# Kernel tuning notes

Hardware: AMD Instinct MI355X
Metric: run time of the kernel (lower is better)

Reference implementation:

```python
import math
import jax, jax.numpy as jnp
import numpy as np

T = 4096
D_MODEL = 1024
NUM_HEADS = 16
HEAD_DIM = D_MODEL // NUM_HEADS


def setup_inputs() -> dict:
    key = jax.random.key(0)
    k_x, k_wqkv, k_wproj = jax.random.split(key, 3)
    # match eqx.nn.Linear init scale: U(-1/sqrt(in), 1/sqrt(in)); randn*small works too,
    # but keep magnitudes reasonable so softmax isn't saturated.
    s_in = 1.0 / math.sqrt(D_MODEL)
    x = jax.random.normal(k_x, (T, D_MODEL), dtype=jnp.float32)
    W_qkv = jax.random.normal(k_wqkv, (3 * D_MODEL, D_MODEL), dtype=jnp.float32) * s_in
    b_qkv = jnp.zeros((3 * D_MODEL,), dtype=jnp.float32)
    W_proj = jax.random.normal(k_wproj, (D_MODEL, D_MODEL), dtype=jnp.float32) * s_in
    b_proj = jnp.zeros((D_MODEL,), dtype=jnp.float32)
    return {"x": x, "W_qkv": W_qkv, "b_qkv": b_qkv, "W_proj": W_proj, "b_proj": b_proj}


def reference(x, W_qkv, b_qkv, W_proj, b_proj):
    T_, C = x.shape  # (seq, d_model)
    H, hd = NUM_HEADS, HEAD_DIM
    # c_attn: eqx Linear computes W @ x + b per token -> x @ W.T + b
    qkv = x @ W_qkv.T + b_qkv  # (T, 3C)
    q, k, v = jnp.split(qkv, 3, axis=1)
    # (T, C) -> (H, T, hd)
    q = q.reshape(T_, H, hd).swapaxes(0, 1)
    k = k.reshape(T_, H, hd).swapaxes(0, 1)
    v = v.reshape(T_, H, hd).swapaxes(0, 1)
    scores = jnp.einsum("htd,hsd->hts", q, k) / math.sqrt(hd)  # (H, T, T)
    causal = jnp.tril(jnp.ones((T_, T_), dtype=bool))
    scores = jnp.where(causal, scores, -jnp.inf)
    attn = jax.nn.softmax(scores, axis=-1)
    y = jnp.einsum("hts,hsd->htd", attn, v)  # (H, T, hd)
    y = y.swapaxes(0, 1).reshape(T_, C)
    y = y @ W_proj.T + b_proj
    return y
```

## Files before the change

kernel.cpp:

```cpp
#include <hip/hip_runtime.h>
#include <math.h>
#include <string.h>

#define T_SEQ 4096
#define DM 1024
#define NH 16
#define HD 64

typedef short s8v __attribute__((ext_vector_type(8)));
typedef float f4v __attribute__((ext_vector_type(4)));

__device__ inline unsigned short f2bf(float f) {
    unsigned u; memcpy(&u, &f, 4);
    u = u + 0x7fffu + ((u >> 16) & 1u);
    return (unsigned short)(u >> 16);
}

__device__ inline float bf2f(unsigned short s) {
    unsigned u = (unsigned)s << 16;
    float f; memcpy(&f, &u, 4);
    return f;
}

__device__ inline float exp2fn(float x) {
#if __has_builtin(__builtin_amdgcn_exp2f)
    return __builtin_amdgcn_exp2f(x);
#else
    return exp2f(x);
#endif
}

__device__ inline void gld_lds16(const void* g, void* l) {
    __builtin_amdgcn_global_load_lds(
        (const __attribute__((address_space(1))) void*)g,
        (__attribute__((address_space(3))) void*)l, 16, 0, 0);
}

__global__ __launch_bounds__(256)
void cvt3(const float* __restrict__ i0, unsigned short* __restrict__ o0, int n0,
          const float* __restrict__ i1, unsigned short* __restrict__ o1, int n1,
          const float* __restrict__ i2, unsigned short* __restrict__ o2, int n2) {
    int i = blockIdx.x * 256 + threadIdx.x;
    const float* in; unsigned short* out; int j;
    if (i < n0)           { in = i0; out = o0; j = i; }
    else if (i < n0 + n1) { in = i1; out = o1; j = i - n0; }
    else if (i < n0 + n1 + n2) { in = i2; out = o2; j = i - n0 - n1; }
    else return;
    const float4* p = (const float4*)(in + (size_t)j * 8);
    float4 a = p[0], b = p[1];
    unsigned short o[8] = {f2bf(a.x), f2bf(a.y), f2bf(a.z), f2bf(a.w),
                           f2bf(b.x), f2bf(b.y), f2bf(b.z), f2bf(b.w)};
    uint4 pk; memcpy(&pk, o, 16);
    *(uint4*)(out + (size_t)j * 8) = pk;
}

template<int MODE, int TN>
__global__ __launch_bounds__(256)
void gemm_bt_mfma(const unsigned short* __restrict__ A, const unsigned short* __restrict__ B,
                  const float* __restrict__ bias, void* __restrict__ Cout,
                  unsigned short* __restrict__ qbuf, unsigned short* __restrict__ kbuf2,
                  unsigned short* __restrict__ vT,
                  int M, int N, int K) {
    constexpr int NF = TN / 32;
    __shared__ __align__(16) short As[4096];
    __shared__ __align__(16) short Bs[TN * 32];
    const int tid = threadIdx.x;
    const int w = tid >> 6, lane = tid & 63;
    const int wr = w >> 1, wc = w & 1;
    const int m0 = blockIdx.y * 128, n0 = blockIdx.x * TN;

    const bool doA = (w < 2);
    const bool doStage = doA || ((w & 1) * 64 < TN);
    const unsigned short* src = doA ? A : B;
    const int rbase = (doA ? m0 : n0) + (w & 1) * 64;
    const unsigned short* gsrc = src + (size_t)(rbase + (lane & 15)) * K + ((lane >> 4) * 8);
    short* ldst = (doA ? As : Bs) + ((w & 1) * 4) * 512;

    f4v acc[4][NF];
    #pragma unroll
    for (int i = 0; i < 4; ++i)
        #pragma unroll
        for (int j = 0; j < NF; ++j) acc[i][j] = (f4v){0.f, 0.f, 0.f, 0.f};

    for (int k0 = 0; k0 < K; k0 += 32) {
        __syncthreads();
        if (doStage) {
            #pragma unroll
            for (int i = 0; i < 4; ++i)
                gld_lds16(gsrc + (size_t)(i * 16) * K + k0, ldst + i * 512);
        }
        __syncthreads();

        s8v af[4], bf[NF];
        #pragma unroll
        for (int i = 0; i < 4; ++i) af[i] = *(const s8v*)&As[((wr * 4 + i) * 64 + lane) * 8];
        #pragma unroll
        for (int j = 0; j < NF; ++j) bf[j] = *(const s8v*)&Bs[((wc * NF + j) * 64 + lane) * 8];
        #pragma unroll
        for (int i = 0; i < 4; ++i)
            #pragma unroll
            for (int j = 0; j < NF; ++j)
                acc[i][j] = __builtin_amdgcn_mfma_f32_16x16x32_bf16(af[i], bf[j], acc[i][j], 0, 0, 0);
    }

    const int l15 = lane & 15, quad = lane >> 4;
    float bj[NF];
    #pragma unroll
    for (int j = 0; j < NF; ++j) bj[j] = bias[n0 + wc * (TN / 2) + j * 16 + l15];

    if (MODE == 2 && n0 >= 2 * DM) {
        const int tile = (m0 + wr * 64) >> 6;
        const int hh = ((n0 - 2 * DM) >> 6) + wc;
        #pragma unroll
        for (int i = 0; i < 4; ++i) {
            #pragma unroll
            for (int j = 0; j < NF; ++j) {
                unsigned short o[4];
                #pragma unroll
                for (int rg = 0; rg < 4; ++rg) o[rg] = f2bf(acc[i][j][rg] + bj[j]);
                unsigned long long pk; memcpy(&pk, o, 8);
                size_t off = (size_t)hh * 262144 + (size_t)tile * 4096
                           + (size_t)((j * 2 + (i >> 1)) * 64 + lane) * 8 + (i & 1) * 4;
                *(unsigned long long*)&vT[off] = pk;
            }
        }
    } else if (MODE == 2) {
        unsigned short* dst = (n0 < DM) ? qbuf : kbuf2;
        const int nb = (n0 < DM) ? n0 : n0 - DM;
        #pragma unroll
        for (int i = 0; i < 4; ++i) {
            #pragma unroll
            for (int rg = 0; rg < 4; ++rg) {
                int row = m0 + wr * 64 + i * 16 + quad * 4 + rg;
                #pragma unroll
                for (int j = 0; j < NF; ++j) {
                    int col = nb + wc * (TN / 2) + j * 16 + l15;
                    dst[(size_t)row * DM + col] = f2bf(acc[i][j][rg] + bj[j]);
                }
            }
        }
    } else {
        #pragma unroll
        for (int i = 0; i < 4; ++i) {
            #pragma unroll
            for (int rg = 0; rg < 4; ++rg) {
                int row = m0 + wr * 64 + i * 16 + quad * 4 + rg;
                #pragma unroll
                for (int j = 0; j < NF; ++j) {
                    int col = n0 + wc * (TN / 2) + j * 16 + l15;
                    ((float*)Cout)[(size_t)row * N + col] = acc[i][j][rg] + bj[j];
                }
            }
        }
    }
}

__device__ __forceinline__ void soft_step(f4v* st, bool diag, int qloc, int quad,
                                          float& lr, s8v& pf0, s8v& pf1) {
    const float C2  = 0.1803368851f;
    const float MC2 = 12.0f * 0.1803368851f;
    float sv[4][4];
    #pragma unroll
    for (int kb = 0; kb < 4; ++kb)
        #pragma unroll
        for (int rg = 0; rg < 4; ++rg) {
            float s = st[kb][rg];
            if (diag && (kb * 16 + quad * 4 + rg > qloc)) s = -3.0e38f;
            float t = exp2fn(fmaf(s, C2, -MC2));
            sv[kb][rg] = t;
            lr += t;
        }
    int pk[4][2];
    #pragma unroll
    for (int kb = 0; kb < 4; ++kb) {
        unsigned u0 = __float_as_uint(sv[kb][0]) + 0x8000u;
        unsigned u1 = __float_as_uint(sv[kb][1]) + 0x8000u;
        unsigned u2 = __float_as_uint(sv[kb][2]) + 0x8000u;
        unsigned u3 = __float_as_uint(sv[kb][3]) + 0x8000u;
        pk[kb][0] = (int)__builtin_amdgcn_perm(u1, u0, 0x07060302);
        pk[kb][1] = (int)__builtin_amdgcn_perm(u3, u2, 0x07060302);
    }
    int4 a = {pk[0][0], pk[0][1], pk[1][0], pk[1][1]};
    int4 b = {pk[2][0], pk[2][1], pk[3][0], pk[3][1]};
    memcpy(&pf0, &a, 16);
    memcpy(&pf1, &b, 16);
}

__global__ __launch_bounds__(256, 3)
void attn_mfma7(const unsigned short* __restrict__ qb,
                const unsigned short* __restrict__ kbf,
                const unsigned short* __restrict__ vT,
                unsigned short* __restrict__ y0,
                unsigned short* __restrict__ y1,
                unsigned short* __restrict__ y2,
                float* __restrict__ lsum) {
    const int b = blockIdx.x;
    const int par = b % 3;
    const int idx = b / 3;
    const int h = idx & 15, a = idx >> 4;
    const int tid = threadIdx.x;
    const int w = tid >> 6, lane = tid & 63;
    const int quad = lane >> 4, l15 = lane & 15;
    const int cq = h * HD;
    unsigned short* ypar = (par == 0) ? y0 : (par == 1) ? y1 : y2;
    float* lpar = lsum + ((size_t)par * NH + h) * T_SEQ;
    const unsigned short* vbase = vT + (size_t)h * 262144;

    __shared__ short KB[2][4096];
    __shared__ short VTs[2][4096];
    __shared__ short QB[8192];

    for (int ph = 0; ph < 2; ++ph) {
        const int qt = ph ? (31 - a) : a;
        const int q0 = qt * 128;
        const int kmax = 2 * qt + 1;
        const int nk = (kmax >= par) ? (kmax - par) / 3 + 1 : 0;
        const int kt0 = par * 64;

        __syncthreads();
        #pragma unroll
        for (int rr = 0; rr < 4; ++rr) {
            int ch = rr * 256 + tid;
            int qg = ch >> 7, hf = (ch >> 6) & 1, ln = ch & 63;
            gld_lds16(qb + (size_t)(q0 + qg * 16 + (ln & 15)) * DM + cq + hf * 32 + ((ln >> 4) << 3),
                      &QB[(ch & ~63) * 8]);
        }
        if (nk > 0) {
            #pragma unroll
            for (int rr = 0; rr < 2; ++rr) {
                int ch = rr * 256 + tid;
                int blk = ch >> 7, hf = (ch >> 6) & 1, ln = ch & 63;
                gld_lds16(kbf + (size_t)(kt0 + blk * 16 + (ln & 15)) * DM + cq + hf * 32 + ((ln >> 4) << 3),
                          &KB[0][(ch & ~63) * 8]);
                gld_lds16(vbase + (size_t)(kt0 >> 6) * 4096 + (size_t)ch * 8,
                          &VTs[0][(ch & ~63) * 8]);
            }
        }
        __syncthreads();

        s8v qf[2][2];
        #pragma unroll
        for (int g = 0; g < 2; ++g)
            #pragma unroll
            for (int hf = 0; hf < 2; ++hf)
                qf[g][hf] = *(const s8v*)&QB[((((g * 4 + w) * 2 + hf) * 64) + lane) * 8];

        f4v O0[4], O1[4];
        #pragma unroll
        for (int ob = 0; ob < 4; ++ob) {
            O0[ob] = (f4v){0.f, 0.f, 0.f, 0.f};
            O1[ob] = (f4v){0.f, 0.f, 0.f, 0.f};
        }
        float lr0 = 0.f, lr1 = 0.f;

        for (int i = 0; i < nk; ++i) {
            const int kt = par + 3 * i;
            const int p = i & 1;
            const bool g0a = (kt <= 2 * qt);
            const bool m0 = (kt == 2 * qt);
            const bool m1 = (kt == 2 * qt + 1);
            if (i < nk - 1) {
                const int k1 = kt0 + (i + 1) * 192;
                #pragma unroll
                for (int rr = 0; rr < 2; ++rr) {
                    int ch = rr * 256 + tid;
                    int blk = ch >> 7, hf = (ch >> 6) & 1, ln = ch & 63;
                    gld_lds16(kbf + (size_t)(k1 + blk * 16 + (ln & 15)) * DM + cq
                                  + hf * 32 + ((ln >> 4) << 3),
                              &KB[p ^ 1][(ch & ~63) * 8]);
                    gld_lds16(vbase + (size_t)(k1 >> 6) * 4096 + (size_t)ch * 8,
                              &VTs[p ^ 1][(ch & ~63) * 8]);
                }
            }

            f4v st0[4], st1[4];
            #pragma unroll
            for (int kb = 0; kb < 4; ++kb) {
                s8v k0f = *(const s8v*)&KB[p][((kb * 2 + 0) * 64 + lane) * 8];
                s8v k1f = *(const s8v*)&KB[p][((kb * 2 + 1) * 64 + lane) * 8];
                f4v c1 = (f4v){0.f, 0.f, 0.f, 0.f};
                c1 = __builtin_amdgcn_mfma_f32_16x16x32_bf16(k0f, qf[1][0], c1, 0, 0, 0);
                c1 = __builtin_amdgcn_mfma_f32_16x16x32_bf16(k1f, qf[1][1], c1, 0, 0, 0);
                st1[kb] = c1;
                if (g0a) {
                    f4v c0 = (f4v){0.f, 0.f, 0.f, 0.f};
                    c0 = __builtin_amdgcn_mfma_f32_16x16x32_bf16(k0f, qf[0][0], c0, 0, 0, 0);
                    c0 = __builtin_amdgcn_mfma_f32_16x16x32_bf16(k1f, qf[0][1], c0, 0, 0, 0);
                    st0[kb] = c0;
                }
            }

            s8v pf10, pf11, pf00, pf01;
            soft_step(st1, m1, w * 16 + l15, quad, lr1, pf10, pf11);
            if (g0a) soft_step(st0, m0, w * 16 + l15, quad, lr0, pf00, pf01);

            #pragma unroll
            for (int ob = 0; ob < 4; ++ob) {
                s8v v0f = *(const s8v*)&VTs[p][((ob * 2 + 0) * 64 + lane) * 8];
                s8v v1f = *(const s8v*)&VTs[p][((ob * 2 + 1) * 64 + lane) * 8];
                O1[ob] = __builtin_amdgcn_mfma_f32_16x16x32_bf16(v0f, pf10, O1[ob], 0, 0, 0);
                O1[ob] = __builtin_amdgcn_mfma_f32_16x16x32_bf16(v1f, pf11, O1[ob], 0, 0, 0);
                if (g0a) {
                    O0[ob] = __builtin_amdgcn_mfma_f32_16x16x32_bf16(v0f, pf00, O0[ob], 0, 0, 0);
                    O0[ob] = __builtin_amdgcn_mfma_f32_16x16x32_bf16(v1f, pf01, O0[ob], 0, 0, 0);
                }
            }
            __syncthreads();
        }

        lr0 += __shfl_xor(lr0, 16); lr0 += __shfl_xor(lr0, 32);
        lr1 += __shfl_xor(lr1, 16); lr1 += __shfl_xor(lr1, 32);
        #pragma unroll
        for (int g = 0; g < 2; ++g) {
            const f4v* O = g ? O1 : O0;
            int qrow = q0 + g * 64 + w * 16 + l15;
            size_t ybase = (size_t)qrow * DM + cq;
            #pragma unroll
            for (int ob = 0; ob < 4; ++ob) {
                unsigned short o[4];
                #pragma unroll
                for (int rg = 0; rg < 4; ++rg) o[rg] = f2bf(O[ob][rg]);
                unsigned long long pk; memcpy(&pk, o, 8);
                *(unsigned long long*)&ypar[ybase + ob * 16 + quad * 4] = pk;
            }
            if (quad == 0) lpar[qrow] = g ? lr1 : lr0;
        }
    }
}

__global__ __launch_bounds__(256)
void attn_combine3(const unsigned short* __restrict__ y0,
                   const unsigned short* __restrict__ y1,
                   const unsigned short* __restrict__ y2,
                   const float* __restrict__ lsum,
                   unsigned short* __restrict__ yout) {
    int i = blockIdx.x * 256 + threadIdx.x;
    int t = i >> 7, d8 = i & 127;
    int h = d8 >> 3;
    float l = lsum[(size_t)h * T_SEQ + t]
            + lsum[((size_t)NH + h) * T_SEQ + t]
            + lsum[((size_t)2 * NH + h) * T_SEQ + t];
    float inv = 1.f / l;
    size_t off = (size_t)t * DM + d8 * 8;
    uint4 ua = *(const uint4*)(y0 + off);
    uint4 ub = *(const uint4*)(y1 + off);
    uint4 uc = *(const uint4*)(y2 + off);
    const unsigned short* pa = (const unsigned short*)&ua;
    const unsigned short* pb = (const unsigned short*)&ub;
    const unsigned short* pc = (const unsigned short*)&uc;
    unsigned short o[8];
    #pragma unroll
    for (int k = 0; k < 8; ++k)
        o[k] = f2bf((bf2f(pa[k]) + bf2f(pb[k]) + bf2f(pc[k])) * inv);
    uint4 pk; memcpy(&pk, o, 16);
    *(uint4*)(yout + off) = pk;
}

extern "C" void kernel_launch(void* const* d_in, const int* in_sizes, int n_in,
                              void* d_out, int out_size, void* d_ws, size_t ws_size,
                              hipStream_t stream) {
    const float* x     = (const float*)d_in[0];
    const float* Wqkv  = (const float*)d_in[1];
    const float* bqkv  = (const float*)d_in[2];
    const float* Wproj = (const float*)d_in[3];
    const float* bproj = (const float*)d_in[4];
    float* out = (float*)d_out;

    char* ws = (char*)d_ws;
    unsigned short* qbuf  = (unsigned short*)(ws);
    unsigned short* kbuf  = (unsigned short*)(ws + ( 8u << 20));
    unsigned short* vTb   = (unsigned short*)(ws + (16u << 20));
    unsigned short* yattb = (unsigned short*)(ws + (24u << 20));
    unsigned short* wprjb = (unsigned short*)(ws + (32u << 20));
    float*          lsum  = (float*)         (ws + (34u << 20));
    unsigned short* xb    = (unsigned short*)(ws + (35u << 20));
    unsigned short* wqkvb = (unsigned short*)(ws + (43u << 20));
    unsigned short* y0p   = (unsigned short*)(ws + (35u << 20));
    unsigned short* y1p   = (unsigned short*)(ws + (43u << 20));
    unsigned short* y2p   = (unsigned short*)(ws + (51u << 20));

    dim3 blk(256);
    {
        int n0 = T_SEQ * DM / 8, n1 = 3 * DM * DM / 8, n2 = DM * DM / 8;
        cvt3<<<dim3((n0 + n1 + n2 + 255) / 256), blk, 0, stream>>>(
            x, xb, n0, Wqkv, wqkvb, n1, Wproj, wprjb, n2);
    }
    gemm_bt_mfma<2, 128><<<dim3(3 * DM / 128, T_SEQ / 128), blk, 0, stream>>>(
        xb, wqkvb, bqkv, nullptr, qbuf, kbuf, vTb, T_SEQ, 3 * DM, DM);
    attn_mfma7<<<dim3(768), blk, 0, stream>>>(qbuf, kbuf, vTb, y0p, y1p, y2p, lsum);
    attn_combine3<<<dim3(T_SEQ * DM / 8 / 256), blk, 0, stream>>>(y0p, y1p, y2p, lsum, yattb);
    gemm_bt_mfma<0, 64><<<dim3(DM / 64, T_SEQ / 128), blk, 0, stream>>>(
        yattb, wprjb, bproj, out, nullptr, nullptr, nullptr, T_SEQ, DM, DM);
}
```

Before: 219.5 us.

## Split attention keys four ways, double-buffer GEMM LDS, compute row sums via MFMA

Several changes land together. The GEMM K-loop now double-buffers its LDS tiles, so the next global-to-LDS load overlaps the current MFMAs and the loop needs one fewer barrier per step. Attention splits each head's keys across four partitions instead of three, giving 1024 blocks, and raises the occupancy hint to 4. Q fragments are now read straight from global memory instead of through LDS, and softmax row sums come from an MFMA against a ones vector rather than scalar adds plus shuffles. The combine kernel sums four partial outputs and writes in place over y0, which costs an extra partial buffer and one more read per element in the combine step.

Result: slower. 251.0 us (+14.4%).

```diff
diff --git a/kernel.cpp b/kernel.cpp
--- a/kernel.cpp
+++ b/kernel.cpp
@@ -62,8 +62,8 @@
                   unsigned short* __restrict__ vT,
                   int M, int N, int K) {
     constexpr int NF = TN / 32;
-    __shared__ __align__(16) short As[4096];
-    __shared__ __align__(16) short Bs[TN * 32];
+    __shared__ __align__(16) short As[2][4096];
+    __shared__ __align__(16) short Bs[2][TN * 32];
     const int tid = threadIdx.x;
     const int w = tid >> 6, lane = tid & 63;
     const int wr = w >> 1, wc = w & 1;
@@ -74,7 +74,7 @@
     const unsigned short* src = doA ? A : B;
     const int rbase = (doA ? m0 : n0) + (w & 1) * 64;
     const unsigned short* gsrc = src + (size_t)(rbase + (lane & 15)) * K + ((lane >> 4) * 8);
-    short* ldst = (doA ? As : Bs) + ((w & 1) * 4) * 512;
+    const int ldoff = ((w & 1) * 4) * 512;
 
     f4v acc[4][NF];
     #pragma unroll
@@ -82,25 +82,34 @@
         #pragma unroll
         for (int j = 0; j < NF; ++j) acc[i][j] = (f4v){0.f, 0.f, 0.f, 0.f};
 
-    for (int k0 = 0; k0 < K; k0 += 32) {
+    auto stage = [&](short* base, int k0) {
+        short* ldst = base + ldoff;
+        #pragma unroll
+        for (int i = 0; i < 4; ++i)
+            gld_lds16(gsrc + (size_t)(i * 16) * K + k0, ldst + i * 512);
+    };
+    auto compute = [&](const short* Ab, const short* Bb) {
+        s8v af[4], bfr[NF];
+        #pragma unroll
+        for (int i = 0; i < 4; ++i) af[i] = *(const s8v*)&Ab[((wr * 4 + i) * 64 + lane) * 8];
+        #pragma unroll
+        for (int j = 0; j < NF; ++j) bfr[j] = *(const s8v*)&Bb[((wc * NF + j) * 64 + lane) * 8];
+        #pragma unroll
+        for (int i = 0; i < 4; ++i)
+            #pragma unroll
+            for (int j = 0; j < NF; ++j)
+                acc[i][j] = __builtin_amdgcn_mfma_f32_16x16x32_bf16(af[i], bfr[j], acc[i][j], 0, 0, 0);
+    };
+
+    if (doStage) stage(doA ? As[0] : Bs[0], 0);
+    __syncthreads();
+    for (int k0 = 0; k0 < K; k0 += 64) {
+        if (doStage) stage(doA ? As[1] : Bs[1], k0 + 32);
+        compute(As[0], Bs[0]);
         __syncthreads();
-        if (doStage) {
-            #pragma unroll
-            for (int i = 0; i < 4; ++i)
-                gld_lds16(gsrc + (size_t)(i * 16) * K + k0, ldst + i * 512);
-        }
+        if (doStage && (k0 + 64 < K)) stage(doA ? As[0] : Bs[0], k0 + 64);
+        compute(As[1], Bs[1]);
         __syncthreads();
-
-        s8v af[4], bf[NF];
-        #pragma unroll
-        for (int i = 0; i < 4; ++i) af[i] = *(const s8v*)&As[((wr * 4 + i) * 64 + lane) * 8];
-        #pragma unroll
-        for (int j = 0; j < NF; ++j) bf[j] = *(const s8v*)&Bs[((wc * NF + j) * 64 + lane) * 8];
-        #pragma unroll
-        for (int i = 0; i < 4; ++i)
-            #pragma unroll
-            for (int j = 0; j < NF; ++j)
-                acc[i][j] = __builtin_amdgcn_mfma_f32_16x16x32_bf16(af[i], bf[j], acc[i][j], 0, 0, 0);
     }
 
     const int l15 = lane & 15, quad = lane >> 4;
@@ -156,7 +165,7 @@
 }
 
 __device__ __forceinline__ void soft_step(f4v* st, bool diag, int qloc, int quad,
-                                          float& lr, s8v& pf0, s8v& pf1) {
+                                          s8v& pf0, s8v& pf1) {
     const float C2  = 0.1803368851f;
     const float MC2 = 12.0f * 0.1803368851f;
     float sv[4][4];
@@ -166,9 +175,7 @@
         for (int rg = 0; rg < 4; ++rg) {
             float s = st[kb][rg];
             if (diag && (kb * 16 + quad * 4 + rg > qloc)) s = -3.0e38f;
-            float t = exp2fn(fmaf(s, C2, -MC2));
-            sv[kb][rg] = t;
-            lr += t;
+            sv[kb][rg] = exp2fn(fmaf(s, C2, -MC2));
         }
     int pk[4][2];
     #pragma unroll
@@ -186,64 +193,62 @@
     memcpy(&pf1, &b, 16);
 }
 
-__global__ __launch_bounds__(256, 3)
-void attn_mfma7(const unsigned short* __restrict__ qb,
+__global__ __launch_bounds__(256, 4)
+void attn_mfma8(const unsigned short* __restrict__ qb,
                 const unsigned short* __restrict__ kbf,
                 const unsigned short* __restrict__ vT,
                 unsigned short* __restrict__ y0,
                 unsigned short* __restrict__ y1,
                 unsigned short* __restrict__ y2,
+                unsigned short* __restrict__ y3,
                 float* __restrict__ lsum) {
     const int b = blockIdx.x;
-    const int par = b % 3;
-    const int idx = b / 3;
+    const int par = b & 3;
+    const int idx = b >> 2;
     const int h = idx & 15, a = idx >> 4;
     const int tid = threadIdx.x;
     const int w = tid >> 6, lane = tid & 63;
     const int quad = lane >> 4, l15 = lane & 15;
     const int cq = h * HD;
-    unsigned short* ypar = (par == 0) ? y0 : (par == 1) ? y1 : y2;
+    unsigned short* ypar = (par == 0) ? y0 : (par == 1) ? y1 : (par == 2) ? y2 : y3;
     float* lpar = lsum + ((size_t)par * NH + h) * T_SEQ;
     const unsigned short* vbase = vT + (size_t)h * 262144;
 
     __shared__ short KB[2][4096];
     __shared__ short VTs[2][4096];
-    __shared__ short QB[8192];
+
+    const s8v onesf = {0x3f80, 0x3f80, 0x3f80, 0x3f80, 0x3f80, 0x3f80, 0x3f80, 0x3f80};
+
+    auto stageKV = [&](int buf, int kk) {
+        #pragma unroll
+        for (int rr = 0; rr < 2; ++rr) {
+            int ch = rr * 256 + tid;
+            int blk = ch >> 7, hf = (ch >> 6) & 1, ln = ch & 63;
+            gld_lds16(kbf + (size_t)(kk + blk * 16 + (ln & 15)) * DM + cq + hf * 32 + ((ln >> 4) << 3),
+                      &KB[buf][(ch & ~63) * 8]);
+            gld_lds16(vbase + (size_t)(kk >> 6) * 4096 + (size_t)ch * 8,
+                      &VTs[buf][(ch & ~63) * 8]);
+        }
+    };
 
     for (int ph = 0; ph < 2; ++ph) {
         const int qt = ph ? (31 - a) : a;
         const int q0 = qt * 128;
         const int kmax = 2 * qt + 1;
-        const int nk = (kmax >= par) ? (kmax - par) / 3 + 1 : 0;
+        const int nk = (kmax >= par) ? (kmax - par) / 4 + 1 : 0;
         const int kt0 = par * 64;
 
         __syncthreads();
-        #pragma unroll
-        for (int rr = 0; rr < 4; ++rr) {
-            int ch = rr * 256 + tid;
-            int qg = ch >> 7, hf = (ch >> 6) & 1, ln = ch & 63;
-            gld_lds16(qb + (size_t)(q0 + qg * 16 + (ln & 15)) * DM + cq + hf * 32 + ((ln >> 4) << 3),
-                      &QB[(ch & ~63) * 8]);
-        }
-        if (nk > 0) {
-            #pragma unroll
-            for (int rr = 0; rr < 2; ++rr) {
-                int ch = rr * 256 + tid;
-                int blk = ch >> 7, hf = (ch >> 6) & 1, ln = ch & 63;
-                gld_lds16(kbf + (size_t)(kt0 + blk * 16 + (ln & 15)) * DM + cq + hf * 32 + ((ln >> 4) << 3),
-                          &KB[0][(ch & ~63) * 8]);
-                gld_lds16(vbase + (size_t)(kt0 >> 6) * 4096 + (size_t)ch * 8,
-                          &VTs[0][(ch & ~63) * 8]);
-            }
-        }
+        if (nk > 0) stageKV(0, kt0);
+
+        s8v qf[2][2];
+        #pragma unroll
+        for (int g = 0; g < 2; ++g)
+            #pragma unroll
+            for (int hf = 0; hf < 2; ++hf)
+                qf[g][hf] = *(const s8v*)&qb[(size_t)(q0 + (g * 4 + w) * 16 + l15) * DM
+                                             + cq + hf * 32 + quad * 8];
         __syncthreads();
-
-        s8v qf[2][2];
-        #pragma unroll
-        for (int g = 0; g < 2; ++g)
-            #pragma unroll
-            for (int hf = 0; hf < 2; ++hf)
-                qf[g][hf] = *(const s8v*)&QB[((((g * 4 + w) * 2 + hf) * 64) + lane) * 8];
 
         f4v O0[4], O1[4];
         #pragma unroll
@@ -251,27 +256,16 @@
             O0[ob] = (f4v){0.f, 0.f, 0.f, 0.f};
             O1[ob] = (f4v){0.f, 0.f, 0.f, 0.f};
         }
-        float lr0 = 0.f, lr1 = 0.f;
+        f4v la0 = (f4v){0.f, 0.f, 0.f, 0.f}, la1 = (f4v){0.f, 0.f, 0.f, 0.f};
 
         for (int i = 0; i < nk; ++i) {
-            const int kt = par + 3 * i;
+            const int kt = par + 4 * i;
             const int p = i & 1;
             const bool g0a = (kt <= 2 * qt);
             const bool m0 = (kt == 2 * qt);
             const bool m1 = (kt == 2 * qt + 1);
-            if (i < nk - 1) {
-                const int k1 = kt0 + (i + 1) * 192;
-                #pragma unroll
-                for (int rr = 0; rr < 2; ++rr) {
-                    int ch = rr * 256 + tid;
-                    int blk = ch >> 7, hf = (ch >> 6) & 1, ln = ch & 63;
-                    gld_lds16(kbf + (size_t)(k1 + blk * 16 + (ln & 15)) * DM + cq
-                                  + hf * 32 + ((ln >> 4) << 3),
-                              &KB[p ^ 1][(ch & ~63) * 8]);
-                    gld_lds16(vbase + (size_t)(k1 >> 6) * 4096 + (size_t)ch * 8,
-                              &VTs[p ^ 1][(ch & ~63) * 8]);
-                }
-            }
+            if (i < nk - 1)
+                stageKV(p ^ 1, kt0 + (i + 1) * 256);
 
             f4v st0[4], st1[4];
             #pragma unroll
@@ -291,8 +285,8 @@
             }
 
             s8v pf10, pf11, pf00, pf01;
-            soft_step(st1, m1, w * 16 + l15, quad, lr1, pf10, pf11);
-            if (g0a) soft_step(st0, m0, w * 16 + l15, quad, lr0, pf00, pf01);
+            soft_step(st1, m1, w * 16 + l15, quad, pf10, pf11);
+            if (g0a) soft_step(st0, m0, w * 16 + l15, quad, pf00, pf01);
 
             #pragma unroll
             for (int ob = 0; ob < 4; ++ob) {
@@ -305,11 +299,16 @@
                     O0[ob] = __builtin_amdgcn_mfma_f32_16x16x32_bf16(v1f, pf01, O0[ob], 0, 0, 0);
                 }
             }
+            la1 = __builtin_amdgcn_mfma_f32_16x16x32_bf16(onesf, pf10, la1, 0, 0, 0);
+            la1 = __builtin_amdgcn_mfma_f32_16x16x32_bf16(onesf, pf11, la1, 0, 0, 0);
+            if (g0a) {
+                la0 = __builtin_amdgcn_mfma_f32_16x16x32_bf16(onesf, pf00, la0, 0, 0, 0);
+                la0 = __builtin_amdgcn_mfma_f32_16x16x32_bf16(onesf, pf01, la0, 0, 0, 0);
+            }
             __syncthreads();
         }
 
-        lr0 += __shfl_xor(lr0, 16); lr0 += __shfl_xor(lr0, 32);
-        lr1 += __shfl_xor(lr1, 16); lr1 += __shfl_xor(lr1, 32);
+        const float lr0 = la0[0], lr1 = la1[0];
         #pragma unroll
         for (int g = 0; g < 2; ++g) {
             const f4v* O = g ? O1 : O0;
@@ -329,9 +328,10 @@
 }
 
 __global__ __launch_bounds__(256)
-void attn_combine3(const unsigned short* __restrict__ y0,
+void attn_combine4(const unsigned short* __restrict__ y0,
                    const unsigned short* __restrict__ y1,
                    const unsigned short* __restrict__ y2,
+                   const unsigned short* __restrict__ y3,
                    const float* __restrict__ lsum,
                    unsigned short* __restrict__ yout) {
     int i = blockIdx.x * 256 + threadIdx.x;
@@ -339,19 +339,22 @@
     int h = d8 >> 3;
     float l = lsum[(size_t)h * T_SEQ + t]
             + lsum[((size_t)NH + h) * T_SEQ + t]
-            + lsum[((size_t)2 * NH + h) * T_SEQ + t];
+            + lsum[((size_t)2 * NH + h) * T_SEQ + t]
+            + lsum[((size_t)3 * NH + h) * T_SEQ + t];
     float inv = 1.f / l;
     size_t off = (size_t)t * DM + d8 * 8;
     uint4 ua = *(const uint4*)(y0 + off);
     uint4 ub = *(const uint4*)(y1 + off);
     uint4 uc = *(const uint4*)(y2 + off);
+    uint4 ud = *(const uint4*)(y3 + off);
     const unsigned short* pa = (const unsigned short*)&ua;
     const unsigned short* pb = (const unsigned short*)&ub;
     const unsigned short* pc = (const unsigned short*)&uc;
+    const unsigned short* pd = (const unsigned short*)&ud;
     unsigned short o[8];
     #pragma unroll
     for (int k = 0; k < 8; ++k)
-        o[k] = f2bf((bf2f(pa[k]) + bf2f(pb[k]) + bf2f(pc[k])) * inv);
+        o[k] = f2bf((bf2f(pa[k]) + bf2f(pb[k]) + bf2f(pc[k]) + bf2f(pd[k])) * inv);
     uint4 pk; memcpy(&pk, o, 16);
     *(uint4*)(yout + off) = pk;
 }
@@ -370,14 +373,14 @@
     unsigned short* qbuf  = (unsigned short*)(ws);
     unsigned short* kbuf  = (unsigned short*)(ws + ( 8u << 20));
     unsigned short* vTb   = (unsigned short*)(ws + (16u << 20));
-    unsigned short* yattb = (unsigned short*)(ws + (24u << 20));
+    unsigned short* y0p   = (unsigned short*)(ws + (24u << 20));
     unsigned short* wprjb = (unsigned short*)(ws + (32u << 20));
     float*          lsum  = (float*)         (ws + (34u << 20));
     unsigned short* xb    = (unsigned short*)(ws + (35u << 20));
     unsigned short* wqkvb = (unsigned short*)(ws + (43u << 20));
-    unsigned short* y0p   = (unsigned short*)(ws + (35u << 20));
-    unsigned short* y1p   = (unsigned short*)(ws + (43u << 20));
-    unsigned short* y2p   = (unsigned short*)(ws + (51u << 20));
+    unsigned short* y1p   = (unsigned short*)(ws + (35u << 20));
+    unsigned short* y2p   = (unsigned short*)(ws + (43u << 20));
+    unsigned short* y3p   = (unsigned short*)(ws + (51u << 20));
 
     dim3 blk(256);
     {
@@ -387,8 +390,8 @@
     }
     gemm_bt_mfma<2, 128><<<dim3(3 * DM / 128, T_SEQ / 128), blk, 0, stream>>>(
         xb, wqkvb, bqkv, nullptr, qbuf, kbuf, vTb, T_SEQ, 3 * DM, DM);
-    attn_mfma7<<<dim3(768), blk, 0, stream>>>(qbuf, kbuf, vTb, y0p, y1p, y2p, lsum);
-    attn_combine3<<<dim3(T_SEQ * DM / 8 / 256), blk, 0, stream>>>(y0p, y1p, y2p, lsum, yattb);
+    attn_mfma8<<<dim3(1024), blk, 0, stream>>>(qbuf, kbuf, vTb, y0p, y1p, y2p, y3p, lsum);
+    attn_combine4<<<dim3(T_SEQ * DM / 8 / 256), blk, 0, stream>>>(y0p, y1p, y2p, y3p, lsum, y0p);
     gemm_bt_mfma<0, 64><<<dim3(DM / 64, T_SEQ / 128), blk, 0, stream>>>(
-        yattb, wprjb, bproj, out, nullptr, nullptr, nullptr, T_SEQ, DM, DM);
-}
+        y0p, wprjb, bproj, out, nullptr, nullptr, nullptr, T_SEQ, DM, DM);
+}
```
